# Performance work log

Hardware: AMD Instinct MI355X
Metric: run time of the kernel (lower is better)

The kernel has to match this reference:

```python
import jax, jax.numpy as jnp
import numpy as np

MIN_NORM = 1e-15
BALL_EPS = 4e-3  # float32 eps used by hgcn PoincareBall.proj
C = 1.0          # curvature


def _artanh(x):
    return jnp.arctanh(jnp.clip(x, -1.0 + 1e-7, 1.0 - 1e-7))


def _norm(x):
    return jnp.clip(jnp.linalg.norm(x, axis=-1, keepdims=True), MIN_NORM)


def proj(x, c):
    n = _norm(x)
    maxn = (1.0 - BALL_EPS) / jnp.sqrt(c)
    return jnp.where(n > maxn, x / n * maxn, x)


def expmap0(u, c):
    sq = jnp.sqrt(c)
    un = _norm(u)
    return jnp.tanh(sq * un) * u / (sq * un)


def logmap0(p, c):
    sq = jnp.sqrt(c)
    pn = _norm(p)
    return _artanh(sq * pn) * p / (sq * pn)


def mobius_add(x, y, c):
    x2 = jnp.sum(x * x, -1, keepdims=True)
    y2 = jnp.sum(y * y, -1, keepdims=True)
    xy = jnp.sum(x * y, -1, keepdims=True)
    num = (1.0 + 2.0 * c * xy + c * y2) * x + (1.0 - c * x2) * y
    den = 1.0 + 2.0 * c * xy + c * c * x2 * y2
    return num / jnp.clip(den, MIN_NORM)


def mobius_matvec(m, x, c):
    sq = jnp.sqrt(c)
    xn = _norm(x)
    mx = x @ m.T  # [N, out]
    mxn = _norm(mx)
    res = jnp.tanh(mxn / xn * _artanh(sq * xn)) * mx / (mxn * sq)
    cond = jnp.all(mx == 0, axis=-1, keepdims=True)
    return jnp.where(cond, jnp.zeros_like(res), res)


def setup_inputs() -> dict:
    key = jax.random.key(0)
    N, D, K, E, DEG = 100000, 512, 16, 3200000, 32
    k1, k2, k3, k4, k5, k6 = jax.random.split(key, 6)
    # valid points on the Poincare ball: expmap0 of small tangent vectors
    x_t = 0.1 * jax.random.normal(k1, (N, D), dtype=jnp.float32)
    x = proj(expmap0(x_t, C), C)
    weight = jax.random.normal(k2, (K, D), dtype=jnp.float32) / np.sqrt(D)
    bias = 0.01 * jax.random.normal(k3, (K,), dtype=jnp.float32)
    # sparse normalized adjacency as edge list
    edge_src = jax.random.randint(k4, (E,), 0, N, dtype=jnp.int64)
    edge_dst = jax.random.randint(k5, (E,), 0, N, dtype=jnp.int64)
    edge_w = jax.random.uniform(k6, (E,), dtype=jnp.float32) / DEG
    return {"x": x, "weight": weight, "bias": bias, "edge_w": edge_w,
            "edge_src": edge_src, "edge_dst": edge_dst}


def reference(x, weight, bias, edge_w, edge_src, edge_dst):
    c = jnp.float32(C)
    n_nodes = x.shape[0]
    # --- HypLinear (dropout=0) ---
    mv = proj(mobius_matvec(weight, x, c), c)                 # [N, K]
    hyp_bias = proj(expmap0(bias[None, :], c), c)             # [1, K]
    h = proj(mobius_add(mv, hyp_bias, c), c)
    # --- HypAgg: aggregate in tangent space at origin via sparse adj ---
    xt = logmap0(h, c)                                        # [N, K]
    msg = edge_w[:, None] * xt[edge_src]                      # [E, K]
    agg = jax.ops.segment_sum(msg, edge_dst, num_segments=n_nodes)
    h = proj(expmap0(agg, c), c)
    # --- HypAct (act = identity, c_in = c_out = c; proj_tan0 is identity) ---
    xt2 = logmap0(h, c)
    h = proj(expmap0(xt2, c), c)
    # --- decode: proj_tan0(logmap0(x, c), c); proj_tan0 identity on the ball ---
    return logmap0(h, c)
```

## Files before the change

kernel.cpp:

```cpp
#include <hip/hip_runtime.h>
#include <hip/hip_fp16.h>
#include <math.h>

#define MIN_NORM 1e-15f
#define MAXN     0.996f
#define ATC      0.9999999f

__device__ __forceinline__ float fast_artanh(float v) {
    v = fminf(fmaxf(v, -ATC), ATC);
    return 0.5f * __logf((1.0f + v) / (1.0f - v));
}
__device__ __forceinline__ float fast_tanh(float xv) {
    float e2 = __expf(2.0f * xv);
    return (e2 - 1.0f) / (e2 + 1.0f);
}
__device__ __forceinline__ float reduce16(float v) {
    v += __shfl_xor(v, 1);
    v += __shfl_xor(v, 2);
    v += __shfl_xor(v, 4);
    v += __shfl_xor(v, 8);
    return v;
}

__global__ __launch_bounds__(256) void hgcn_k1(
    const float* __restrict__ x, const float* __restrict__ weight,
    const float* __restrict__ bias, _Float16* __restrict__ xt, int N)
{
    const int tid  = threadIdx.x;
    const int lane = tid & 63;
    const int wib  = tid >> 6;
    const int k    = lane & 15;
    const int grp  = lane >> 4;

    float wr[16][8];
    const float* wp = weight + lane * 8;
#pragma unroll
    for (int kk = 0; kk < 16; ++kk) {
        float4 a = *(const float4*)(wp + kk * 512);
        float4 b = *(const float4*)(wp + kk * 512 + 4);
        wr[kk][0] = a.x; wr[kk][1] = a.y; wr[kk][2] = a.z; wr[kk][3] = a.w;
        wr[kk][4] = b.x; wr[kk][5] = b.y; wr[kk][6] = b.z; wr[kk][7] = b.w;
    }

    float bb = bias[k];
    float b2 = reduce16(bb * bb);
    float bn = fmaxf(sqrtf(b2), MIN_NORM);
    float eb = fast_tanh(bn) * bb / bn;
    float e2 = reduce16(eb * eb);
    float en = fmaxf(sqrtf(e2), MIN_NORM);
    float hb = (en > MAXN) ? eb * (MAXN / en) : eb;
    float y2 = reduce16(hb * hb);

    const long long stride = (long long)gridDim.x * 16;
    long long base = ((long long)blockIdx.x * 4 + wib) * 4;

    float4 c0 = {0,0,0,0}, c1 = {0,0,0,0};
    float4 n0 = {0,0,0,0}, n1 = {0,0,0,0};
    if (base < N) {
        const float* xr = x + base * 512 + lane * 8;
        c0 = *(const float4*)(xr);
        c1 = *(const float4*)(xr + 4);
    }
    if (base + 1 < N) {
        const float* xr = x + (base + 1) * 512 + lane * 8;
        n0 = *(const float4*)(xr);
        n1 = *(const float4*)(xr + 4);
    }

    while (base < N) {
        float x2sel = 0.0f, mxsel = 0.0f;

#pragma unroll
        for (int p = 0; p < 4; ++p) {
            long long r2 = (p < 2) ? (base + p + 2) : (base + stride + (p - 2));
            float4 m0 = {0,0,0,0}, m1 = {0,0,0,0};
            if (r2 < N) {
                const float* xr = x + r2 * 512 + lane * 8;
                m0 = *(const float4*)(xr);
                m1 = *(const float4*)(xr + 4);
            }

            float xv[8] = {c0.x, c0.y, c0.z, c0.w, c1.x, c1.y, c1.z, c1.w};

            float pq = 0.0f;
#pragma unroll
            for (int jj = 0; jj < 8; ++jj) pq = fmaf(xv[jj], xv[jj], pq);
#pragma unroll
            for (int m = 1; m <= 32; m <<= 1) pq += __shfl_xor(pq, m);
            if (grp == p) x2sel = pq;

            float v8[8];
            {
                const bool h = lane & 1;
#pragma unroll
                for (int i = 0; i < 8; ++i) {
                    float a0 = 0.0f, a1 = 0.0f;
#pragma unroll
                    for (int jj = 0; jj < 8; ++jj) {
                        a0 = fmaf(wr[2*i][jj],   xv[jj], a0);
                        a1 = fmaf(wr[2*i+1][jj], xv[jj], a1);
                    }
                    float keep = h ? a1 : a0;
                    float give = h ? a0 : a1;
                    v8[i] = keep + __shfl_xor(give, 1);
                }
            }
            float v4[4];
            {
                const bool h = lane & 2;
#pragma unroll
                for (int i = 0; i < 4; ++i) {
                    float keep = h ? v8[2*i+1] : v8[2*i];
                    float give = h ? v8[2*i]   : v8[2*i+1];
                    v4[i] = keep + __shfl_xor(give, 2);
                }
            }
            float v2[2];
            {
                const bool h = lane & 4;
#pragma unroll
                for (int i = 0; i < 2; ++i) {
                    float keep = h ? v4[2*i+1] : v4[2*i];
                    float give = h ? v4[2*i]   : v4[2*i+1];
                    v2[i] = keep + __shfl_xor(give, 4);
                }
            }
            float mx;
            {
                const bool h = lane & 8;
                float keep = h ? v2[1] : v2[0];
                float give = h ? v2[0] : v2[1];
                mx = keep + __shfl_xor(give, 8);
            }
            mx += __shfl_xor(mx, 16);
            mx += __shfl_xor(mx, 32);
            if (grp == p) mxsel = mx;

            c0 = n0; c1 = n1;
            n0 = m0; n1 = m1;
        }

        float mx2 = reduce16(mxsel * mxsel);
        float xn  = fmaxf(sqrtf(x2sel), MIN_NORM);
        float mxn = fmaxf(sqrtf(mx2),   MIN_NORM);
        float res = fast_tanh(mxn / xn * fast_artanh(xn)) * mxsel / mxn;
        if (mx2 == 0.0f) res = 0.0f;
        float rn2 = reduce16(res * res);
        float rn  = fmaxf(sqrtf(rn2), MIN_NORM);
        float mv  = (rn > MAXN) ? res * (MAXN / rn) : res;
        float mv2 = reduce16(mv * mv);
        float xy  = reduce16(mv * hb);
        float num = (1.0f + 2.0f * xy + y2) * mv + (1.0f - mv2) * hb;
        float den = 1.0f + 2.0f * xy + mv2 * y2;
        float hq  = num / fmaxf(den, MIN_NORM);
        float hn2 = reduce16(hq * hq);
        float hn  = fmaxf(sqrtf(hn2), MIN_NORM);
        float hp  = (hn > MAXN) ? hq * (MAXN / hn) : hq;
        float hp2 = reduce16(hp * hp);
        float pn  = fmaxf(sqrtf(hp2), MIN_NORM);
        float xtv = fast_artanh(pn) * hp / pn;

        long long myrow = base + grp;
        if (myrow < N) xt[myrow * 16 + k] = (_Float16)xtv;

        base += stride;
    }
}

__global__ void hgcn_k_detect(const void* srcp, long long E, int* flag)
{
    const int tid = threadIdx.x;
    if (tid == 0) *flag = 0;
    __syncthreads();
    long long n = E / 2; if (n > 4096) n = 4096;
    int bad = 0;
    const unsigned long long* p = (const unsigned long long*)srcp;
    for (long long i = tid; i < n; i += 256)
        if (p[i] >= (1ULL << 32)) bad = 1;
    if (bad) atomicOr(flag, 1);
}

__global__ __launch_bounds__(256) void hgcn_k2(
    const void* __restrict__ srcp, const void* __restrict__ dstp,
    const float* __restrict__ ew, const _Float16* __restrict__ xt,
    __half2* __restrict__ aggh, long long E, const int* __restrict__ flag)
{
    const int sub = threadIdx.x & 7;
    const bool i32 = (*flag != 0);
    const long long slots = ((long long)gridDim.x * 256) >> 3;
    long long e = ((long long)blockIdx.x * 256 + threadIdx.x) >> 3;

    long long d0 = 0; float w0 = 0.0f; __half2 v0 = __floats2half2_rn(0.f, 0.f);
    bool have = e < E;
    if (have) {
        long long s0;
        if (i32) { s0 = __builtin_nontemporal_load((const int*)srcp + e);
                   d0 = __builtin_nontemporal_load((const int*)dstp + e); }
        else     { s0 = __builtin_nontemporal_load((const long long*)srcp + e);
                   d0 = __builtin_nontemporal_load((const long long*)dstp + e); }
        w0 = __builtin_nontemporal_load(ew + e);
        v0 = *(const __half2*)(xt + s0 * 16 + sub * 2);
    }
    while (have) {
        long long en = e + slots;
        long long d1 = 0; float w1 = 0.0f; __half2 v1 = __floats2half2_rn(0.f, 0.f);
        bool haven = en < E;
        if (haven) {
            long long s1;
            if (i32) { s1 = __builtin_nontemporal_load((const int*)srcp + en);
                       d1 = __builtin_nontemporal_load((const int*)dstp + en); }
            else     { s1 = __builtin_nontemporal_load((const long long*)srcp + en);
                       d1 = __builtin_nontemporal_load((const long long*)dstp + en); }
            w1 = __builtin_nontemporal_load(ew + en);
            v1 = *(const __half2*)(xt + s1 * 16 + sub * 2);
        }
        __half2 contrib = __floats2half2_rn(w0 * __low2float(v0),
                                            w0 * __high2float(v0));
        unsafeAtomicAdd(&aggh[d0 * 8 + sub], contrib);
        e = en; d0 = d1; w0 = w1; v0 = v1; have = haven;
    }
}

__global__ __launch_bounds__(256) void hgcn_k3(
    const __half* __restrict__ aggh, float* __restrict__ out, int N)
{
    int gid = blockIdx.x * blockDim.x + threadIdx.x;
    int row = gid >> 4;
    if (row >= N) return;
    float u = __half2float(aggh[(size_t)row * 16 + (gid & 15)]);

    float un2 = reduce16(u * u);
    float un  = fmaxf(sqrtf(un2), MIN_NORM);
    float h1  = fast_tanh(un) * u / un;
    float n2  = reduce16(h1 * h1);
    float n1  = fmaxf(sqrtf(n2), MIN_NORM);
    float h1p = (n1 > MAXN) ? h1 * (MAXN / n1) : h1;
    float m2  = reduce16(h1p * h1p);
    float pn  = fmaxf(sqrtf(m2), MIN_NORM);
    float xt2 = fast_artanh(pn) * h1p / pn;
    float a2  = reduce16(xt2 * xt2);
    float an  = fmaxf(sqrtf(a2), MIN_NORM);
    float h2  = fast_tanh(an) * xt2 / an;
    float b2  = reduce16(h2 * h2);
    float bn  = fmaxf(sqrtf(b2), MIN_NORM);
    float h2p = (bn > MAXN) ? h2 * (MAXN / bn) : h2;
    float c2  = reduce16(h2p * h2p);
    float cn  = fmaxf(sqrtf(c2), MIN_NORM);
    out[(size_t)row * 16 + (gid & 15)] = fast_artanh(cn) * h2p / cn;
}

extern "C" void kernel_launch(void* const* d_in, const int* in_sizes, int n_in,
                              void* d_out, int out_size, void* d_ws, size_t ws_size,
                              hipStream_t stream)
{
    const float* x        = (const float*)d_in[0];
    const float* weight   = (const float*)d_in[1];
    const float* bias     = (const float*)d_in[2];
    const float* edge_w   = (const float*)d_in[3];
    const void*  edge_src = d_in[4];
    const void*  edge_dst = d_in[5];

    const int Kv = in_sizes[2];
    const int Dv = in_sizes[1] / Kv;
    const int N  = in_sizes[0] / Dv;
    const long long E = in_sizes[3];

    int*      flag = (int*)d_ws;
    _Float16* xt   = (_Float16*)((char*)d_ws + 256);
    __half2*  aggh = (__half2*)((char*)d_ws + 256 + (size_t)N * 16 * sizeof(_Float16));

    (void)hipMemsetAsync(aggh, 0, (size_t)N * 16 * sizeof(__half), stream);
    hipLaunchKernelGGL(hgcn_k_detect, dim3(1), dim3(256), 0, stream, edge_src, E, flag);
    hipLaunchKernelGGL(hgcn_k1, dim3(1024), dim3(256), 0, stream,
                       x, weight, bias, xt, N);
    hipLaunchKernelGGL(hgcn_k2, dim3(2048), dim3(256), 0, stream,
                       edge_src, edge_dst, edge_w, xt, aggh, E, flag);
    hipLaunchKernelGGL(hgcn_k3, dim3((unsigned)(((long long)N * 16 + 255) / 256)), dim3(256), 0, stream,
                       (const __half*)aggh, (float*)d_out, N);
}
```

Before: 260.2 us.

## Stage x rows via async global-to-LDS loads and fold detect into k1

```diff
diff --git a/kernel.cpp b/kernel.cpp
--- a/kernel.cpp
+++ b/kernel.cpp
@@ -22,15 +22,40 @@
     return v;
 }
 
+__device__ __forceinline__ void stage_row(const float* __restrict__ xrow,
+                                          float* ldsslot) {
+    const int lane = threadIdx.x & 63;
+    const char* g = (const char*)xrow + lane * 16;
+    char* l = (char*)ldsslot;
+    __builtin_amdgcn_global_load_lds(
+        (const __attribute__((address_space(1))) void*)g,
+        (__attribute__((address_space(3))) void*)l, 16, 0, 0);
+    __builtin_amdgcn_global_load_lds(
+        (const __attribute__((address_space(1))) void*)(g + 1024),
+        (__attribute__((address_space(3))) void*)(l + 1024), 16, 0, 0);
+}
+
 __global__ __launch_bounds__(256) void hgcn_k1(
     const float* __restrict__ x, const float* __restrict__ weight,
-    const float* __restrict__ bias, _Float16* __restrict__ xt, int N)
-{
+    const float* __restrict__ bias, _Float16* __restrict__ xt, int N,
+    const void* __restrict__ srcp, long long E, int* __restrict__ flag)
+{
+    __shared__ float lds[4][4][512];
     const int tid  = threadIdx.x;
     const int lane = tid & 63;
     const int wib  = tid >> 6;
     const int k    = lane & 15;
     const int grp  = lane >> 4;
+
+    if (blockIdx.x == 0 && wib == 0) {
+        long long n = E / 2; if (n > 4096) n = 4096;
+        bool bad = false;
+        const unsigned long long* p = (const unsigned long long*)srcp;
+        for (long long i = lane; i < n; i += 64)
+            if (p[i] >= (1ULL << 32)) bad = true;
+        unsigned long long m = __ballot(bad);
+        if (lane == 0) *flag = (m != 0ULL) ? 1 : 0;
+    }
 
     float wr[16][8];
     const float* wp = weight + lane * 8;
@@ -53,34 +78,31 @@
 
     const long long stride = (long long)gridDim.x * 16;
     long long base = ((long long)blockIdx.x * 4 + wib) * 4;
-
-    float4 c0 = {0,0,0,0}, c1 = {0,0,0,0};
-    float4 n0 = {0,0,0,0}, n1 = {0,0,0,0};
-    if (base < N) {
-        const float* xr = x + base * 512 + lane * 8;
-        c0 = *(const float4*)(xr);
-        c1 = *(const float4*)(xr + 4);
-    }
-    if (base + 1 < N) {
-        const float* xr = x + (base + 1) * 512 + lane * 8;
-        n0 = *(const float4*)(xr);
-        n1 = *(const float4*)(xr + 4);
-    }
-
-    while (base < N) {
+    if (base >= N) return;
+
+    asm volatile("s_waitcnt vmcnt(0)" ::: "memory");
+#pragma unroll
+    for (int p = 0; p < 4; ++p) {
+        long long r = base + p;
+        stage_row(x + (r < N ? r : 0) * 512, &lds[wib][p][0]);
+    }
+
+    for (long long gb = base; gb < N; gb += stride) {
         float x2sel = 0.0f, mxsel = 0.0f;
 
 #pragma unroll
         for (int p = 0; p < 4; ++p) {
-            long long r2 = (p < 2) ? (base + p + 2) : (base + stride + (p - 2));
-            float4 m0 = {0,0,0,0}, m1 = {0,0,0,0};
-            if (r2 < N) {
-                const float* xr = x + r2 * 512 + lane * 8;
-                m0 = *(const float4*)(xr);
-                m1 = *(const float4*)(xr + 4);
-            }
-
-            float xv[8] = {c0.x, c0.y, c0.z, c0.w, c1.x, c1.y, c1.z, c1.w};
+            asm volatile("s_waitcnt vmcnt(6)" ::: "memory");
+            __builtin_amdgcn_sched_barrier(0);
+            const float4* sp = (const float4*)&lds[wib][p][0];
+            float4 a = sp[lane * 2];
+            float4 b = sp[lane * 2 + 1];
+            asm volatile("s_waitcnt lgkmcnt(0)" ::: "memory");
+            __builtin_amdgcn_sched_barrier(0);
+            long long rn = gb + stride + p;
+            stage_row(x + (rn < N ? rn : 0) * 512, &lds[wib][p][0]);
+
+            float xv[8] = {a.x, a.y, a.z, a.w, b.x, b.y, b.z, b.w};
 
             float pq = 0.0f;
 #pragma unroll
@@ -135,9 +157,6 @@
             mx += __shfl_xor(mx, 16);
             mx += __shfl_xor(mx, 32);
             if (grp == p) mxsel = mx;
-
-            c0 = n0; c1 = n1;
-            n0 = m0; n1 = m1;
         }
 
         float mx2 = reduce16(mxsel * mxsel);
@@ -160,24 +179,9 @@
         float pn  = fmaxf(sqrtf(hp2), MIN_NORM);
         float xtv = fast_artanh(pn) * hp / pn;
 
-        long long myrow = base + grp;
+        long long myrow = gb + grp;
         if (myrow < N) xt[myrow * 16 + k] = (_Float16)xtv;
-
-        base += stride;
-    }
-}
-
-__global__ void hgcn_k_detect(const void* srcp, long long E, int* flag)
-{
-    const int tid = threadIdx.x;
-    if (tid == 0) *flag = 0;
-    __syncthreads();
-    long long n = E / 2; if (n > 4096) n = 4096;
-    int bad = 0;
-    const unsigned long long* p = (const unsigned long long*)srcp;
-    for (long long i = tid; i < n; i += 256)
-        if (p[i] >= (1ULL << 32)) bad = 1;
-    if (bad) atomicOr(flag, 1);
+    }
 }
 
 __global__ __launch_bounds__(256) void hgcn_k2(
@@ -270,9 +274,8 @@
     __half2*  aggh = (__half2*)((char*)d_ws + 256 + (size_t)N * 16 * sizeof(_Float16));
 
     (void)hipMemsetAsync(aggh, 0, (size_t)N * 16 * sizeof(__half), stream);
-    hipLaunchKernelGGL(hgcn_k_detect, dim3(1), dim3(256), 0, stream, edge_src, E, flag);
-    hipLaunchKernelGGL(hgcn_k1, dim3(1024), dim3(256), 0, stream,
-                       x, weight, bias, xt, N);
+    hipLaunchKernelGGL(hgcn_k1, dim3(512), dim3(256), 0, stream,
+                       x, weight, bias, xt, N, edge_src, E, flag);
     hipLaunchKernelGGL(hgcn_k2, dim3(2048), dim3(256), 0, stream,
                        edge_src, edge_dst, edge_w, xt, aggh, E, flag);
     hipLaunchKernelGGL(hgcn_k3, dim3((unsigned)(((long long)N * 16 + 255) / 256)), dim3(256), 0, stream,
```

After: 270.6 us. 1.04x slower.
